# Optimization experiments

Hardware: AMD Instinct MI355X
Metric: run time of the kernel (lower is better)

The kernel has to match this reference:

```python
import jax, jax.numpy as jnp
import numpy as np

B, S, E, H, D = 4, 2048, 1024, 16, 64   # batch, seq, embed, heads, head_dim
NUM_BUCKETS, MAX_DISTANCE = 32, 128


def _relative_position_bucket(relative_position, num_buckets, max_distance):
    # causal T5-style bucketing
    max_exact = num_buckets // 2
    max_distance = max(max_distance, max_exact + 1)
    distance = jnp.maximum(-relative_position, 0)
    is_small = distance < max_exact
    safe_distance = jnp.maximum(distance, 1)
    log_scale = jnp.log(safe_distance / max_exact) / jnp.log(max_distance / max_exact)
    large_bucket = max_exact + (log_scale * (num_buckets - max_exact)).astype(jnp.int32)
    large_bucket = jnp.minimum(large_bucket, num_buckets - 1)
    return jnp.where(is_small, distance, large_bucket)


def setup_inputs() -> dict:
    key = jax.random.key(0)
    ks = jax.random.split(key, 7)
    w_scale = 1.0 / np.sqrt(E)
    inputs_q = jax.random.normal(ks[0], (B, S, E), jnp.float32)
    inputs_kv = jax.random.normal(ks[1], (B, S, E), jnp.float32)
    Wq = jax.random.normal(ks[2], (E, H * D), jnp.float32) * w_scale
    Wk = jax.random.normal(ks[3], (E, H * D), jnp.float32) * w_scale
    Wv = jax.random.normal(ks[4], (E, H * D), jnp.float32) * w_scale
    Wo = jax.random.normal(ks[5], (H * D, E), jnp.float32) * (1.0 / np.sqrt(H * D))
    rel_bias = jax.random.normal(ks[6], (H, NUM_BUCKETS), jnp.float32) * 0.02
    mask = jnp.tril(jnp.ones((S, S), dtype=bool))[None, None]  # [1,1,Q,K] causal
    return {"inputs_q": inputs_q, "inputs_kv": inputs_kv, "mask": mask,
            "Wq": Wq, "Wk": Wk, "Wv": Wv, "Wo": Wo, "rel_bias": rel_bias}


def reference(inputs_q, inputs_kv, mask, Wq, Wk, Wv, Wo, rel_bias):
    batch, q_len, embed = inputs_q.shape
    k_len = inputs_kv.shape[1]
    q = (inputs_q @ Wq).reshape(batch, q_len, H, D)
    k = (inputs_kv @ Wk).reshape(batch, k_len, H, D)
    v = (inputs_kv @ Wv).reshape(batch, k_len, H, D)
    attention = jnp.einsum("bqhd,bkhd->bhqk", q, k) * (1.0 / jnp.sqrt(D))
    # T5 relative position bias
    rel_pos = jnp.arange(k_len, dtype=jnp.int32)[None, :] - jnp.arange(q_len, dtype=jnp.int32)[:, None]
    bucket = _relative_position_bucket(rel_pos, NUM_BUCKETS, MAX_DISTANCE)  # [Q,K]
    attention = attention + jnp.take(rel_bias, bucket, axis=1)[None]  # [1,H,Q,K]
    attention = jnp.where(mask, attention, jnp.finfo(jnp.float32).min)
    normalized = jax.nn.softmax(attention, axis=-1)
    output = jnp.einsum("bhqk,bkhd->bqhd", normalized, v).reshape(batch, q_len, H * D)
    return output @ Wo
```

## Files before the change

kernel.cpp:

```cpp
#include <hip/hip_runtime.h>

typedef unsigned short u16;
typedef unsigned int u32;
typedef __bf16 bf16x8 __attribute__((ext_vector_type(8)));
typedef float f32x4 __attribute__((ext_vector_type(4)));
typedef float f32x16 __attribute__((ext_vector_type(16)));

#define S_LEN 2048
#define EMB 1024
#define NH 16
#define HD 64
#define LOG2E 1.44269504088896f

__device__ __forceinline__ u16 f2bf(float f) {
  union { float f; unsigned u; } v; v.f = f;
  unsigned r = (v.u + 0x7fffu + ((v.u >> 16) & 1u)) >> 16;
  return (u16)r;
}

__device__ __forceinline__ u32 packbf(float a, float b) {
  union { __bf16 h[2]; u32 u; } x;
  x.h[0] = (__bf16)a; x.h[1] = (__bf16)b;
  return x.u;
}

__device__ __forceinline__ void g2l16(const void* g, void* l) {
  __builtin_amdgcn_global_load_lds(
      (const unsigned int __attribute__((address_space(1)))*)g,
      (unsigned int __attribute__((address_space(3)))*)l, 16, 0, 0);
}

__device__ __forceinline__ void permswap_f(float a, float b, float& x, float& y) {
  auto r = __builtin_amdgcn_permlane32_swap(__float_as_int(a), __float_as_int(b), false, false);
  x = __int_as_float(r[0]);
  y = __int_as_float(r[1]);
}


__global__ void cvt_bf16(const float* __restrict__ src, u16* __restrict__ dst, int n4) {
  int i = blockIdx.x * blockDim.x + threadIdx.x;
  if (i < n4) {
    float4 f = ((const float4*)src)[i];
    ushort4 o;
    o.x = f2bf(f.x); o.y = f2bf(f.y); o.z = f2bf(f.z); o.w = f2bf(f.w);
    ((ushort4*)dst)[i] = o;
  }
}

__global__ void transcvt(const float* __restrict__ W, u16* __restrict__ Wt) {
  __shared__ float t[32][33];
  int k0 = blockIdx.x * 32, n0 = blockIdx.y * 32;
  int tx = threadIdx.x & 31, ty = threadIdx.x >> 5;
#pragma unroll
  for (int i = 0; i < 4; i++) t[ty + i * 8][tx] = W[(k0 + ty + i * 8) * 1024 + n0 + tx];
  __syncthreads();
#pragma unroll
  for (int i = 0; i < 4; i++) Wt[(n0 + ty + i * 8) * 1024 + k0 + tx] = f2bf(t[tx][ty + i * 8]);
}

__global__ void build_bias(const float* __restrict__ rel, float* __restrict__ tbl) {
  int i = blockIdx.x * 256 + threadIdx.x;
  int h = i >> 11, dist = i & 2047;
  int bk;
  if (dist < 16) {
    bk = dist;
  } else {
    float ls = logf((float)dist * (1.0f / 16.0f)) * (1.0f / logf(8.0f));
    bk = 16 + (int)(ls * 16.0f);
    if (bk > 31) bk = 31;
  }
  tbl[i] = rel[h * 32 + bk];
}


template <int MODE>
__global__ __launch_bounds__(256, 2) void gemm_bf16(const u16* __restrict__ A,
                                                    const u16* __restrict__ Bt,
                                                    void* __restrict__ C, float scale) {
  constexpr int K = EMB;
  __shared__ u16 As[2][128 * 32];
  __shared__ u16 Bs[2][128 * 32];
  const int m0 = blockIdx.y * 128;
  const int n0 = blockIdx.x * 128;
  const int tid = threadIdx.x;
  const int lane = tid & 63;
  const int wid = tid >> 6;
  const int wm = (wid >> 1) * 64;
  const int wn = (wid & 1) * 64;
  const int la = lane & 15;
  const int lg = lane >> 4;

  const int r0 = tid >> 2;
  const int c0 = ((tid & 3) ^ (r0 & 3)) * 8;
  const u16* gA = A + (size_t)(m0 + r0) * K + c0;
  const u16* gB = Bt + (size_t)(n0 + r0) * K + c0;

  f32x4 acc[4][4] = {};

  g2l16(gA, As[0] + tid * 8);
  g2l16(gA + 64 * K, As[0] + tid * 8 + 2048);
  g2l16(gB, Bs[0] + tid * 8);
  g2l16(gB + 64 * K, Bs[0] + tid * 8 + 2048);
  gA += 32;
  gB += 32;

  for (int t = 0; t < 32; ++t) {
    const int cur = t & 1;
    if (t < 31) {
      u16* lA = As[cur ^ 1] + tid * 8;
      u16* lB = Bs[cur ^ 1] + tid * 8;
      g2l16(gA, lA);
      g2l16(gA + 64 * K, lA + 2048);
      g2l16(gB, lB);
      g2l16(gB + 64 * K, lB + 2048);
      gA += 32;
      gB += 32;
      asm volatile("s_waitcnt vmcnt(4)" ::: "memory");
    } else {
      asm volatile("s_waitcnt vmcnt(0)" ::: "memory");
    }
    __builtin_amdgcn_s_barrier();
    asm volatile("" ::: "memory");

    bf16x8 af[4], bb[4];
#pragma unroll
    for (int mf = 0; mf < 4; mf++) {
      int row = wm + mf * 16 + la;
      af[mf] = *(const bf16x8*)&As[cur][row * 32 + ((lg ^ (row & 3)) << 3)];
    }
#pragma unroll
    for (int nf = 0; nf < 4; nf++) {
      int row = wn + nf * 16 + la;
      bb[nf] = *(const bf16x8*)&Bs[cur][row * 32 + ((lg ^ (row & 3)) << 3)];
    }
#pragma unroll
    for (int mf = 0; mf < 4; mf++)
#pragma unroll
      for (int nf = 0; nf < 4; nf++)
        acc[mf][nf] =
            __builtin_amdgcn_mfma_f32_16x16x32_bf16(af[mf], bb[nf], acc[mf][nf], 0, 0, 0);

    asm volatile("" ::: "memory");
    __builtin_amdgcn_s_barrier();
    asm volatile("" ::: "memory");
  }

#pragma unroll
  for (int mf = 0; mf < 4; mf++)
#pragma unroll
    for (int nf = 0; nf < 4; nf++)
#pragma unroll
      for (int r = 0; r < 4; r++) {
        int m = m0 + wm + mf * 16 + lg * 4 + r;
        int n = n0 + wn + nf * 16 + la;
        float v = acc[mf][nf][r] * scale;
        if constexpr (MODE == 0) {
          int b = m >> 11, s = m & 2047, h = n >> 6, d = n & 63;
          ((u16*)C)[(((size_t)(b * 16 + h) * 2048 + s) << 6) + d] = f2bf(v);
        } else if constexpr (MODE == 1) {
          int b = m >> 11, s = m & 2047, h = n >> 6, d = n & 63;
          ((u16*)C)[(((size_t)(b * 16 + h) * 64 + d) << 11) + s] = f2bf(v);
        } else {
          ((float*)C)[(size_t)m * 1024 + n] = v;
        }
      }
}


__global__ __launch_bounds__(256, 2) void attn_kernel(const u16* __restrict__ Qb,
                                                      const u16* __restrict__ Kb,
                                                      const u16* __restrict__ Vtb,
                                                      const float* __restrict__ btbl,
                                                      u16* __restrict__ O) {
  __shared__ u16 Ks[2][64 * 64];
  __shared__ u16 Vs[2][64 * 64];
  __shared__ float bias_s[S_LEN];

  const int bh = blockIdx.x;
  const int h = bh & (NH - 1);
  const int b = bh >> 4;
  const int qt = 15 - blockIdx.y;
  const int q0 = qt * 128;
  const int tid = threadIdx.x;
  const int lane = tid & 63;
  const int w = tid >> 6;
  const int la = lane & 31;
  const int hi = lane >> 5;

  {
    const float4* src = (const float4*)(btbl + h * S_LEN);
    float4* dst = (float4*)bias_s;
    dst[tid] = src[tid];
    dst[tid + 256] = src[tid + 256];
  }

  const u16* Qg = Qb + (size_t)bh * S_LEN * HD;
  const u16* Kg = Kb + (size_t)bh * S_LEN * HD;
  const u16* Vg = Vtb + (size_t)bh * HD * S_LEN;

  const int qw = q0 + w * 32;
  const int q = qw + la;

  bf16x8 qfrag[4];
#pragma unroll
  for (int kk = 0; kk < 4; kk++)
    qfrag[kk] = *(const bf16x8*)&Qg[(size_t)q * HD + kk * 16 + hi * 8];

  f32x16 oacc[2] = {};
  float mrun = -1e30f;
  float lrun = 0.f;

  const int sr = tid >> 3;
  const int scz = ((tid & 7) ^ (sr & 7)) * 8;
  const u16* kp = Kg + sr * 64 + scz;
  const u16* vp = Vg + (size_t)sr * S_LEN + scz;

  const int ntblk = (q0 + 128) >> 6;
  const int qmax = qw + 31;

  g2l16(kp, Ks[0] + tid * 8);
  g2l16(kp + 32 * 64, Ks[0] + tid * 8 + 2048);
  g2l16(vp, Vs[0] + tid * 8);
  g2l16(vp + 32 * S_LEN, Vs[0] + tid * 8 + 2048);
  kp += 4096;
  vp += 64;
  __syncthreads();

  const float bias31 = bias_s[S_LEN - 1];

  for (int t = 0; t < ntblk; ++t) {
    const int cur = t & 1;
    if (t + 1 < ntblk) {
      u16* lK = Ks[cur ^ 1] + tid * 8;
      u16* lV = Vs[cur ^ 1] + tid * 8;
      g2l16(kp, lK);
      g2l16(kp + 32 * 64, lK + 2048);
      g2l16(vp, lV);
      g2l16(vp + 32 * S_LEN, lV + 2048);
      kp += 4096;
      vp += 64;
      asm volatile("s_waitcnt vmcnt(4)" ::: "memory");
    } else {
      asm volatile("s_waitcnt vmcnt(0)" ::: "memory");
    }
    __builtin_amdgcn_s_barrier();
    asm volatile("" ::: "memory");

    const int kv0 = t << 6;
    if (kv0 <= qmax) {
      f32x16 sacc[2] = {};
      __builtin_amdgcn_s_setprio(1);
#pragma unroll
      for (int kk = 0; kk < 4; kk++) {
#pragma unroll
        for (int nf = 0; nf < 2; nf++) {
          int row = nf * 32 + la;
          bf16x8 kf = *(const bf16x8*)&Ks[cur][row * 64 + (((kk * 2 + hi) ^ (row & 7)) << 3)];
          sacc[nf] = __builtin_amdgcn_mfma_f32_32x32x16_bf16(kf, qfrag[kk], sacc[nf], 0, 0, 0);
        }
      }
      __builtin_amdgcn_s_setprio(0);

      float pf[32];
      float adde = 0.f;
      if (kv0 + 176 <= qw) {
#pragma unroll
        for (int nf = 0; nf < 2; nf++)
#pragma unroll
          for (int r = 0; r < 16; r++) pf[nf * 16 + r] = sacc[nf][r];
        adde = bias31;
      } else {
        const int qb2 = q - kv0 - 4 * hi;
        const float* bp = bias_s + (qb2 - 59);
        if (kv0 + 63 <= qw) {
#pragma unroll
          for (int nf = 0; nf < 2; nf++)
#pragma unroll
            for (int r = 0; r < 16; r++) {
              const int Cn = nf * 32 + (r & 3) + ((r >> 2) << 3);
              pf[nf * 16 + r] = sacc[nf][r] + bp[59 - Cn];
            }
        } else {
#pragma unroll
          for (int nf = 0; nf < 2; nf++)
#pragma unroll
            for (int r = 0; r < 16; r++) {
              const int Cn = nf * 32 + (r & 3) + ((r >> 2) << 3);
              pf[nf * 16 + r] = (Cn <= qb2) ? (sacc[nf][r] + bp[59 - Cn]) : -1e30f;
            }
        }
      }

      float a[11];
#pragma unroll
      for (int i = 0; i < 10; i++)
        a[i] = fmaxf(fmaxf(pf[3 * i], pf[3 * i + 1]), pf[3 * i + 2]);
      a[10] = fmaxf(pf[30], pf[31]);
      float b0 = fmaxf(fmaxf(a[0], a[1]), a[2]);
      float b1 = fmaxf(fmaxf(a[3], a[4]), a[5]);
      float b2 = fmaxf(fmaxf(a[6], a[7]), a[8]);
      float b3 = fmaxf(a[9], a[10]);
      float mt = fmaxf(fmaxf(b0, b1), fmaxf(b2, b3)) + adde;
      {
        float x, y;
        permswap_f(mt, mt, x, y);
        mt = fmaxf(x, y);
      }

      if (__any(mt > mrun + 8.0f)) {
        float mn = fmaxf(mrun, mt);
        float sc = exp2f((mrun - mn) * LOG2E);
        mrun = mn;
        lrun *= sc;
        oacc[0] *= sc;
        oacc[1] *= sc;
      }
      const float ec = (adde - mrun) * LOG2E;

      float ps[16];
#pragma unroll
      for (int i = 0; i < 16; i++) {
        float p0 = exp2f(fmaf(pf[i], LOG2E, ec));
        float p1 = exp2f(fmaf(pf[i + 16], LOG2E, ec));
        pf[i] = p0;
        pf[i + 16] = p1;
        ps[i] = p0 + p1;
      }
#pragma unroll
      for (int i = 0; i < 8; i++) ps[i] += ps[i + 8];
#pragma unroll
      for (int i = 0; i < 4; i++) ps[i] += ps[i + 4];
      float rs = (ps[0] + ps[1]) + (ps[2] + ps[3]);
      {
        float x, y;
        permswap_f(rs, rs, x, y);
        rs = x + y;
      }
      lrun += rs;

      u32 paw[4][4];
#pragma unroll
      for (int ks = 0; ks < 4; ks++) {
        const int nf = ks >> 1;
        const int e80 = (ks & 1) * 2;
#pragma unroll
        for (int half = 0; half < 2; half++) {
          u32 Y0 = packbf(pf[nf * 16 + 4 * e80 + 2 * half], pf[nf * 16 + 4 * e80 + 2 * half + 1]);
          u32 Y1 = packbf(pf[nf * 16 + 4 * (e80 + 1) + 2 * half],
                          pf[nf * 16 + 4 * (e80 + 1) + 2 * half + 1]);
          auto r = __builtin_amdgcn_permlane32_swap((int)Y0, (int)Y1, false, false);
          paw[ks][half] = (u32)r[0];
          paw[ks][2 + half] = (u32)r[1];
        }
      }

      __builtin_amdgcn_s_setprio(1);
#pragma unroll
      for (int d2 = 0; d2 < 2; d2++) {
#pragma unroll
        for (int ks = 0; ks < 4; ks++) {
          int row = d2 * 32 + la;
          bf16x8 vf = *(const bf16x8*)&Vs[cur][row * 64 + (((ks * 2 + hi) ^ (row & 7)) << 3)];
          union { u32 w[4]; bf16x8 v; } pu;
          pu.w[0] = paw[ks][0]; pu.w[1] = paw[ks][1];
          pu.w[2] = paw[ks][2]; pu.w[3] = paw[ks][3];
          oacc[d2] = __builtin_amdgcn_mfma_f32_32x32x16_bf16(vf, pu.v, oacc[d2], 0, 0, 0);
        }
      }
      __builtin_amdgcn_s_setprio(0);
    }

    asm volatile("" ::: "memory");
    __builtin_amdgcn_s_barrier();
    asm volatile("" ::: "memory");
  }

  const float inv = 1.0f / lrun;
  u16* Og = O + ((size_t)(b * S_LEN + q)) * EMB + h * HD;
#pragma unroll
  for (int d2 = 0; d2 < 2; d2++)
#pragma unroll
    for (int g = 0; g < 4; g++) {
      ushort4 ov;
      ov.x = f2bf(oacc[d2][g * 4 + 0] * inv);
      ov.y = f2bf(oacc[d2][g * 4 + 1] * inv);
      ov.z = f2bf(oacc[d2][g * 4 + 2] * inv);
      ov.w = f2bf(oacc[d2][g * 4 + 3] * inv);
      *(ushort4*)&Og[d2 * 32 + g * 8 + hi * 4] = ov;
    }
}


extern "C" void kernel_launch(void* const* d_in, const int* in_sizes, int n_in, void* d_out,
                              int out_size, void* d_ws, size_t ws_size, hipStream_t stream) {
  (void)in_sizes; (void)n_in; (void)out_size; (void)ws_size;
  const float* inq = (const float*)d_in[0];
  const float* inkv = (const float*)d_in[1];
  const float* Wq = (const float*)d_in[3];
  const float* Wk = (const float*)d_in[4];
  const float* Wv = (const float*)d_in[5];
  const float* Wo = (const float*)d_in[6];
  const float* rel = (const float*)d_in[7];
  float* out = (float*)d_out;

  char* ws = (char*)d_ws;
  size_t off = 0;
  auto alloc = [&](size_t bytes) {
    void* p = ws + off;
    off += (bytes + 255) & ~(size_t)255;
    return p;
  };
  u16* Aq = (u16*)alloc(16777216);
  u16* Akv = (u16*)alloc(16777216);
  u16* Wqt = (u16*)alloc(2097152);
  u16* Wkt = (u16*)alloc(2097152);
  u16* Wvt = (u16*)alloc(2097152);
  u16* Wot = (u16*)alloc(2097152);
  u16* Qb = (u16*)alloc(16777216);
  u16* Kb = (u16*)alloc(16777216);
  u16* Vtb = (u16*)alloc(16777216);
  u16* Ob = (u16*)alloc(16777216);
  float* btbl = (float*)alloc(131072);

  cvt_bf16<<<8192, 256, 0, stream>>>(inq, Aq, 2097152);
  cvt_bf16<<<8192, 256, 0, stream>>>(inkv, Akv, 2097152);
  transcvt<<<dim3(32, 32), 256, 0, stream>>>(Wq, Wqt);
  transcvt<<<dim3(32, 32), 256, 0, stream>>>(Wk, Wkt);
  transcvt<<<dim3(32, 32), 256, 0, stream>>>(Wv, Wvt);
  transcvt<<<dim3(32, 32), 256, 0, stream>>>(Wo, Wot);
  build_bias<<<128, 256, 0, stream>>>(rel, btbl);

  gemm_bf16<0><<<dim3(8, 64), 256, 0, stream>>>(Aq, Wqt, Qb, 0.125f);
  gemm_bf16<0><<<dim3(8, 64), 256, 0, stream>>>(Akv, Wkt, Kb, 1.0f);
  gemm_bf16<1><<<dim3(8, 64), 256, 0, stream>>>(Akv, Wvt, Vtb, 1.0f);
  attn_kernel<<<dim3(64, 16), 256, 0, stream>>>(Qb, Kb, Vtb, btbl, Ob);
  gemm_bf16<2><<<dim3(8, 64), 256, 0, stream>>>(Ob, Wot, out, 1.0f);
}
```

Measured before the change: 225.8 us.

## Fuse QKV GEMMs, fold log2e into scales, packed softmax, unroll attention loop

The three Q/K/V projection GEMMs become a single launch over concatenated transposed weights, which fills more of the GPU in one grid. The softmax scale and the bias table are pre-multiplied by log2e so the exponentials need no extra FMA, the rescale threshold is adjusted to match, and the softmax reductions use packed two-wide float ops. The attention tile loop is manually unrolled by two with compile-time buffer indices. The GEMMs drop their double-buffered LDS prefetch for a simple single-buffer load-then-sync loop, which may expose global-load latency.

```diff
diff --git a/kernel.cpp b/kernel.cpp
--- a/kernel.cpp
+++ b/kernel.cpp
@@ -3,6 +3,7 @@
 typedef unsigned short u16;
 typedef unsigned int u32;
 typedef __bf16 bf16x8 __attribute__((ext_vector_type(8)));
+typedef float f32x2 __attribute__((ext_vector_type(2)));
 typedef float f32x4 __attribute__((ext_vector_type(4)));
 typedef float f32x16 __attribute__((ext_vector_type(16)));
 
@@ -11,6 +12,8 @@
 #define NH 16
 #define HD 64
 #define LOG2E 1.44269504088896f
+#define QSCALE (0.125f * LOG2E)
+#define THRL 11.5415603f
 
 __device__ __forceinline__ u16 f2bf(float f) {
   union { float f; unsigned u; } v; v.f = f;
@@ -30,10 +33,13 @@
       (unsigned int __attribute__((address_space(3)))*)l, 16, 0, 0);
 }
 
-__device__ __forceinline__ void permswap_f(float a, float b, float& x, float& y) {
-  auto r = __builtin_amdgcn_permlane32_swap(__float_as_int(a), __float_as_int(b), false, false);
-  x = __int_as_float(r[0]);
-  y = __int_as_float(r[1]);
+__device__ __forceinline__ float permswap_max(float a) {
+  auto r = __builtin_amdgcn_permlane32_swap(__float_as_int(a), __float_as_int(a), false, false);
+  return fmaxf(__int_as_float(r[0]), __int_as_float(r[1]));
+}
+__device__ __forceinline__ float permswap_add(float a) {
+  auto r = __builtin_amdgcn_permlane32_swap(__float_as_int(a), __float_as_int(a), false, false);
+  return __int_as_float(r[0]) + __int_as_float(r[1]);
 }
 
 
@@ -69,17 +75,92 @@
     bk = 16 + (int)(ls * 16.0f);
     if (bk > 31) bk = 31;
   }
-  tbl[i] = rel[h * 32 + bk];
-}
-
-
-template <int MODE>
-__global__ __launch_bounds__(256, 2) void gemm_bf16(const u16* __restrict__ A,
-                                                    const u16* __restrict__ Bt,
-                                                    void* __restrict__ C, float scale) {
+  tbl[i] = rel[h * 32 + bk] * LOG2E;
+}
+
+
+__global__ __launch_bounds__(256, 2) void gemm_qkv(const u16* __restrict__ Aq,
+                                                   const u16* __restrict__ Akv,
+                                                   const u16* __restrict__ Wt,
+                                                   u16* __restrict__ QKV, float qscale) {
   constexpr int K = EMB;
-  __shared__ u16 As[2][128 * 32];
-  __shared__ u16 Bs[2][128 * 32];
+  __shared__ u16 As[128 * 32];
+  __shared__ u16 Bs[128 * 32];
+  const int m0 = blockIdx.y * 128;
+  const int n0 = blockIdx.x * 128;
+  const int mat = n0 >> 10;
+  const u16* A = (mat == 0) ? Aq : Akv;
+  const int tid = threadIdx.x;
+  const int lane = tid & 63;
+  const int wid = tid >> 6;
+  const int wm = (wid >> 1) * 64;
+  const int wn = (wid & 1) * 64;
+  const int la = lane & 15;
+  const int lg = lane >> 4;
+
+  const int r0 = tid >> 2;
+  const int c0 = ((tid & 3) ^ (r0 & 3)) * 8;
+  const u16* gA = A + (size_t)(m0 + r0) * K + c0;
+  const u16* gB = Wt + (size_t)(n0 + r0) * K + c0;
+  u16* lA = As + tid * 8;
+  u16* lB = Bs + tid * 8;
+
+  f32x4 acc[4][4] = {};
+
+  for (int k0 = 0; k0 < K; k0 += 32) {
+    g2l16(gA, lA);
+    g2l16(gA + 64 * K, lA + 2048);
+    g2l16(gB, lB);
+    g2l16(gB + 64 * K, lB + 2048);
+    gA += 32;
+    gB += 32;
+    __syncthreads();
+    bf16x8 af[4], bb[4];
+#pragma unroll
+    for (int mf = 0; mf < 4; mf++) {
+      int row = wm + mf * 16 + la;
+      af[mf] = *(const bf16x8*)&As[row * 32 + ((lg ^ (row & 3)) << 3)];
+    }
+#pragma unroll
+    for (int nf = 0; nf < 4; nf++) {
+      int row = wn + nf * 16 + la;
+      bb[nf] = *(const bf16x8*)&Bs[row * 32 + ((lg ^ (row & 3)) << 3)];
+    }
+#pragma unroll
+    for (int mf = 0; mf < 4; mf++)
+#pragma unroll
+      for (int nf = 0; nf < 4; nf++)
+        acc[mf][nf] =
+            __builtin_amdgcn_mfma_f32_16x16x32_bf16(af[mf], bb[nf], acc[mf][nf], 0, 0, 0);
+    __syncthreads();
+  }
+
+  const float sc = (mat == 0) ? qscale : 1.0f;
+#pragma unroll
+  for (int mf = 0; mf < 4; mf++)
+#pragma unroll
+    for (int nf = 0; nf < 4; nf++)
+#pragma unroll
+      for (int r = 0; r < 4; r++) {
+        int m = m0 + wm + mf * 16 + lg * 4 + r;
+        int n = n0 + wn + nf * 16 + la;
+        float v = acc[mf][nf][r] * sc;
+        int b = m >> 11, s = m & 2047, h = (n >> 6) & 15, d = n & 63;
+        size_t base = (size_t)mat << 23;
+        if (mat < 2)
+          QKV[base + (((size_t)(b * 16 + h) * 2048 + s) << 6) + d] = f2bf(v);
+        else
+          QKV[base + (((size_t)(b * 16 + h) * 64 + d) << 11) + s] = f2bf(v);
+      }
+}
+
+
+__global__ __launch_bounds__(256, 2) void gemm_out(const u16* __restrict__ A,
+                                                   const u16* __restrict__ Bt,
+                                                   float* __restrict__ C) {
+  constexpr int K = EMB;
+  __shared__ u16 As[128 * 32];
+  __shared__ u16 Bs[128 * 32];
   const int m0 = blockIdx.y * 128;
   const int n0 = blockIdx.x * 128;
   const int tid = threadIdx.x;
@@ -94,44 +175,29 @@
   const int c0 = ((tid & 3) ^ (r0 & 3)) * 8;
   const u16* gA = A + (size_t)(m0 + r0) * K + c0;
   const u16* gB = Bt + (size_t)(n0 + r0) * K + c0;
+  u16* lA = As + tid * 8;
+  u16* lB = Bs + tid * 8;
 
   f32x4 acc[4][4] = {};
 
-  g2l16(gA, As[0] + tid * 8);
-  g2l16(gA + 64 * K, As[0] + tid * 8 + 2048);
-  g2l16(gB, Bs[0] + tid * 8);
-  g2l16(gB + 64 * K, Bs[0] + tid * 8 + 2048);
-  gA += 32;
-  gB += 32;
-
-  for (int t = 0; t < 32; ++t) {
-    const int cur = t & 1;
-    if (t < 31) {
-      u16* lA = As[cur ^ 1] + tid * 8;
-      u16* lB = Bs[cur ^ 1] + tid * 8;
-      g2l16(gA, lA);
-      g2l16(gA + 64 * K, lA + 2048);
-      g2l16(gB, lB);
-      g2l16(gB + 64 * K, lB + 2048);
-      gA += 32;
-      gB += 32;
-      asm volatile("s_waitcnt vmcnt(4)" ::: "memory");
-    } else {
-      asm volatile("s_waitcnt vmcnt(0)" ::: "memory");
-    }
-    __builtin_amdgcn_s_barrier();
-    asm volatile("" ::: "memory");
-
+  for (int k0 = 0; k0 < K; k0 += 32) {
+    g2l16(gA, lA);
+    g2l16(gA + 64 * K, lA + 2048);
+    g2l16(gB, lB);
+    g2l16(gB + 64 * K, lB + 2048);
+    gA += 32;
+    gB += 32;
+    __syncthreads();
     bf16x8 af[4], bb[4];
 #pragma unroll
     for (int mf = 0; mf < 4; mf++) {
       int row = wm + mf * 16 + la;
-      af[mf] = *(const bf16x8*)&As[cur][row * 32 + ((lg ^ (row & 3)) << 3)];
+      af[mf] = *(const bf16x8*)&As[row * 32 + ((lg ^ (row & 3)) << 3)];
     }
 #pragma unroll
     for (int nf = 0; nf < 4; nf++) {
       int row = wn + nf * 16 + la;
-      bb[nf] = *(const bf16x8*)&Bs[cur][row * 32 + ((lg ^ (row & 3)) << 3)];
+      bb[nf] = *(const bf16x8*)&Bs[row * 32 + ((lg ^ (row & 3)) << 3)];
     }
 #pragma unroll
     for (int mf = 0; mf < 4; mf++)
@@ -139,10 +205,7 @@
       for (int nf = 0; nf < 4; nf++)
         acc[mf][nf] =
             __builtin_amdgcn_mfma_f32_16x16x32_bf16(af[mf], bb[nf], acc[mf][nf], 0, 0, 0);
-
-    asm volatile("" ::: "memory");
-    __builtin_amdgcn_s_barrier();
-    asm volatile("" ::: "memory");
+    __syncthreads();
   }
 
 #pragma unroll
@@ -153,19 +216,155 @@
       for (int r = 0; r < 4; r++) {
         int m = m0 + wm + mf * 16 + lg * 4 + r;
         int n = n0 + wn + nf * 16 + la;
-        float v = acc[mf][nf][r] * scale;
-        if constexpr (MODE == 0) {
-          int b = m >> 11, s = m & 2047, h = n >> 6, d = n & 63;
-          ((u16*)C)[(((size_t)(b * 16 + h) * 2048 + s) << 6) + d] = f2bf(v);
-        } else if constexpr (MODE == 1) {
-          int b = m >> 11, s = m & 2047, h = n >> 6, d = n & 63;
-          ((u16*)C)[(((size_t)(b * 16 + h) * 64 + d) << 11) + s] = f2bf(v);
-        } else {
-          ((float*)C)[(size_t)m * 1024 + n] = v;
-        }
+        C[(size_t)m * 1024 + n] = acc[mf][nf][r];
       }
 }
 
+
+__device__ __forceinline__ void softmax_repack(const f32x16* sacc, int kv0, int qw, int q, int hi,
+                                               const float* bias_s, float bias31, float& mrun,
+                                               float& lrun, f32x16& o0, f32x16& o1,
+                                               u32 (&paw)[4][4]) {
+  f32x2 pf[16];
+  float adde = 0.f;
+  if (kv0 + 176 <= qw) {
+#pragma unroll
+    for (int j = 0; j < 16; j++) {
+      const int nf = j >> 3, r = (j & 7) * 2;
+      pf[j] = (f32x2){sacc[nf][r], sacc[nf][r + 1]};
+    }
+    adde = bias31;
+  } else {
+    const int qb2 = q - kv0 - 4 * hi;
+    const float* bp = bias_s + (qb2 - 59);
+    if (kv0 + 63 <= qw) {
+#pragma unroll
+      for (int j = 0; j < 16; j++) {
+        const int nf = j >> 3, r = (j & 7) * 2;
+        const int Cn = nf * 32 + (r & 3) + ((r >> 2) << 3);
+        f32x2 bv = {bp[59 - Cn], bp[58 - Cn]};
+        pf[j] = (f32x2){sacc[nf][r], sacc[nf][r + 1]} + bv;
+      }
+    } else {
+#pragma unroll
+      for (int j = 0; j < 16; j++) {
+        const int nf = j >> 3, r = (j & 7) * 2;
+        const int Cn = nf * 32 + (r & 3) + ((r >> 2) << 3);
+        pf[j].x = (Cn <= qb2) ? (sacc[nf][r] + bp[59 - Cn]) : -1e30f;
+        pf[j].y = (Cn + 1 <= qb2) ? (sacc[nf][r + 1] + bp[58 - Cn]) : -1e30f;
+      }
+    }
+  }
+
+  f32x2 t8[8];
+#pragma unroll
+  for (int i = 0; i < 8; i++) t8[i] = __builtin_elementwise_max(pf[i], pf[i + 8]);
+#pragma unroll
+  for (int i = 0; i < 4; i++) t8[i] = __builtin_elementwise_max(t8[i], t8[i + 4]);
+  f32x2 m2 = __builtin_elementwise_max(__builtin_elementwise_max(t8[0], t8[1]),
+                                       __builtin_elementwise_max(t8[2], t8[3]));
+  float mt = fmaxf(m2.x, m2.y) + adde;
+  mt = permswap_max(mt);
+
+  if (__any(mt > mrun + THRL)) {
+    float mn = fmaxf(mrun, mt);
+    float s = exp2f(mrun - mn);
+    mrun = mn;
+    lrun *= s;
+    o0 *= s;
+    o1 *= s;
+  }
+  const f32x2 ec2 = {adde - mrun, adde - mrun};
+
+  f32x2 s8[8];
+#pragma unroll
+  for (int j = 0; j < 16; j++) {
+    f32x2 a = pf[j] + ec2;
+    f32x2 p = {exp2f(a.x), exp2f(a.y)};
+    pf[j] = p;
+    if (j < 8) s8[j] = p;
+    else s8[j - 8] += p;
+  }
+#pragma unroll
+  for (int i = 0; i < 4; i++) s8[i] += s8[i + 4];
+  f32x2 s2 = (s8[0] + s8[1]) + (s8[2] + s8[3]);
+  lrun += permswap_add(s2.x + s2.y);
+
+#pragma unroll
+  for (int ks = 0; ks < 4; ks++) {
+    const int j0b = (ks >> 1) * 8 + (ks & 1) * 4;
+#pragma unroll
+    for (int half = 0; half < 2; half++) {
+      u32 Y0 = packbf(pf[j0b + half].x, pf[j0b + half].y);
+      u32 Y1 = packbf(pf[j0b + 2 + half].x, pf[j0b + 2 + half].y);
+      auto r = __builtin_amdgcn_permlane32_swap((int)Y0, (int)Y1, false, false);
+      paw[ks][half] = (u32)r[0];
+      paw[ks][2 + half] = (u32)r[1];
+    }
+  }
+}
+
+template <int CUR>
+__device__ __forceinline__ void tile_body(int t, int ntblk, int qmax, int qw, int q, int hi,
+                                          int la, int tid, const u16*& kp, const u16*& vp,
+                                          u16 (*Ks)[64 * 64], u16 (*Vs)[64 * 64],
+                                          const bf16x8 (&qfrag)[4], const float* bias_s,
+                                          float bias31, float& mrun, float& lrun, f32x16& o0,
+                                          f32x16& o1) {
+  if (t + 1 < ntblk) {
+    u16* lK = Ks[CUR ^ 1] + tid * 8;
+    u16* lV = Vs[CUR ^ 1] + tid * 8;
+    g2l16(kp, lK);
+    g2l16(kp + 32 * 64, lK + 2048);
+    g2l16(vp, lV);
+    g2l16(vp + 32 * S_LEN, lV + 2048);
+    kp += 4096;
+    vp += 64;
+    asm volatile("s_waitcnt vmcnt(4)" ::: "memory");
+  } else {
+    asm volatile("s_waitcnt vmcnt(0)" ::: "memory");
+  }
+  __builtin_amdgcn_s_barrier();
+  asm volatile("" ::: "memory");
+
+  const int kv0 = t << 6;
+  if (kv0 <= qmax) {
+    f32x16 sacc[2] = {};
+    __builtin_amdgcn_s_setprio(1);
+#pragma unroll
+    for (int kk = 0; kk < 4; kk++)
+#pragma unroll
+      for (int nf = 0; nf < 2; nf++) {
+        int row = nf * 32 + la;
+        bf16x8 kf = *(const bf16x8*)&Ks[CUR][row * 64 + (((kk * 2 + hi) ^ (row & 7)) << 3)];
+        sacc[nf] = __builtin_amdgcn_mfma_f32_32x32x16_bf16(kf, qfrag[kk], sacc[nf], 0, 0, 0);
+      }
+    __builtin_amdgcn_s_setprio(0);
+
+    u32 paw[4][4];
+    softmax_repack(sacc, kv0, qw, q, hi, bias_s, bias31, mrun, lrun, o0, o1, paw);
+
+    __builtin_amdgcn_s_setprio(1);
+#pragma unroll
+    for (int d2 = 0; d2 < 2; d2++) {
+      f32x16& oa = d2 ? o1 : o0;
+#pragma unroll
+      for (int ks = 0; ks < 4; ks++) {
+        int row = d2 * 32 + la;
+        bf16x8 vf = *(const bf16x8*)&Vs[CUR][row * 64 + (((ks * 2 + hi) ^ (row & 7)) << 3)];
+        union { u32 w[4]; bf16x8 v; } pu;
+        pu.w[0] = paw[ks][0]; pu.w[1] = paw[ks][1];
+        pu.w[2] = paw[ks][2]; pu.w[3] = paw[ks][3];
+        oa = __builtin_amdgcn_mfma_f32_32x32x16_bf16(vf, pu.v, oa, 0, 0, 0);
+      }
+    }
+    __builtin_amdgcn_s_setprio(0);
+  }
+
+  asm volatile("" ::: "memory");
+  __builtin_amdgcn_s_barrier();
+  asm volatile("" ::: "memory");
+}
 
 __global__ __launch_bounds__(256, 2) void attn_kernel(const u16* __restrict__ Qb,
                                                       const u16* __restrict__ Kb,
@@ -206,7 +405,7 @@
   for (int kk = 0; kk < 4; kk++)
     qfrag[kk] = *(const bf16x8*)&Qg[(size_t)q * HD + kk * 16 + hi * 8];
 
-  f32x16 oacc[2] = {};
+  f32x16 o0 = {}, o1 = {};
   float mrun = -1e30f;
   float lrun = 0.f;
 
@@ -224,170 +423,37 @@
   g2l16(vp + 32 * S_LEN, Vs[0] + tid * 8 + 2048);
   kp += 4096;
   vp += 64;
-  __syncthreads();
+  asm volatile("s_waitcnt lgkmcnt(0)" ::: "memory");
+  __builtin_amdgcn_s_barrier();
+  asm volatile("" ::: "memory");
 
   const float bias31 = bias_s[S_LEN - 1];
 
-  for (int t = 0; t < ntblk; ++t) {
-    const int cur = t & 1;
-    if (t + 1 < ntblk) {
-      u16* lK = Ks[cur ^ 1] + tid * 8;
-      u16* lV = Vs[cur ^ 1] + tid * 8;
-      g2l16(kp, lK);
-      g2l16(kp + 32 * 64, lK + 2048);
-      g2l16(vp, lV);
-      g2l16(vp + 32 * S_LEN, lV + 2048);
-      kp += 4096;
-      vp += 64;
-      asm volatile("s_waitcnt vmcnt(4)" ::: "memory");
-    } else {
-      asm volatile("s_waitcnt vmcnt(0)" ::: "memory");
-    }
-    __builtin_amdgcn_s_barrier();
-    asm volatile("" ::: "memory");
-
-    const int kv0 = t << 6;
-    if (kv0 <= qmax) {
-      f32x16 sacc[2] = {};
-      __builtin_amdgcn_s_setprio(1);
-#pragma unroll
-      for (int kk = 0; kk < 4; kk++) {
-#pragma unroll
-        for (int nf = 0; nf < 2; nf++) {
-          int row = nf * 32 + la;
-          bf16x8 kf = *(const bf16x8*)&Ks[cur][row * 64 + (((kk * 2 + hi) ^ (row & 7)) << 3)];
-          sacc[nf] = __builtin_amdgcn_mfma_f32_32x32x16_bf16(kf, qfrag[kk], sacc[nf], 0, 0, 0);
-        }
-      }
-      __builtin_amdgcn_s_setprio(0);
-
-      float pf[32];
-      float adde = 0.f;
-      if (kv0 + 176 <= qw) {
-#pragma unroll
-        for (int nf = 0; nf < 2; nf++)
-#pragma unroll
-          for (int r = 0; r < 16; r++) pf[nf * 16 + r] = sacc[nf][r];
-        adde = bias31;
-      } else {
-        const int qb2 = q - kv0 - 4 * hi;
-        const float* bp = bias_s + (qb2 - 59);
-        if (kv0 + 63 <= qw) {
-#pragma unroll
-          for (int nf = 0; nf < 2; nf++)
-#pragma unroll
-            for (int r = 0; r < 16; r++) {
-              const int Cn = nf * 32 + (r & 3) + ((r >> 2) << 3);
-              pf[nf * 16 + r] = sacc[nf][r] + bp[59 - Cn];
-            }
-        } else {
-#pragma unroll
-          for (int nf = 0; nf < 2; nf++)
-#pragma unroll
-            for (int r = 0; r < 16; r++) {
-              const int Cn = nf * 32 + (r & 3) + ((r >> 2) << 3);
-              pf[nf * 16 + r] = (Cn <= qb2) ? (sacc[nf][r] + bp[59 - Cn]) : -1e30f;
-            }
-        }
-      }
-
-      float a[11];
-#pragma unroll
-      for (int i = 0; i < 10; i++)
-        a[i] = fmaxf(fmaxf(pf[3 * i], pf[3 * i + 1]), pf[3 * i + 2]);
-      a[10] = fmaxf(pf[30], pf[31]);
-      float b0 = fmaxf(fmaxf(a[0], a[1]), a[2]);
-      float b1 = fmaxf(fmaxf(a[3], a[4]), a[5]);
-      float b2 = fmaxf(fmaxf(a[6], a[7]), a[8]);
-      float b3 = fmaxf(a[9], a[10]);
-      float mt = fmaxf(fmaxf(b0, b1), fmaxf(b2, b3)) + adde;
-      {
-        float x, y;
-        permswap_f(mt, mt, x, y);
-        mt = fmaxf(x, y);
-      }
-
-      if (__any(mt > mrun + 8.0f)) {
-        float mn = fmaxf(mrun, mt);
-        float sc = exp2f((mrun - mn) * LOG2E);
-        mrun = mn;
-        lrun *= sc;
-        oacc[0] *= sc;
-        oacc[1] *= sc;
-      }
-      const float ec = (adde - mrun) * LOG2E;
-
-      float ps[16];
-#pragma unroll
-      for (int i = 0; i < 16; i++) {
-        float p0 = exp2f(fmaf(pf[i], LOG2E, ec));
-        float p1 = exp2f(fmaf(pf[i + 16], LOG2E, ec));
-        pf[i] = p0;
-        pf[i + 16] = p1;
-        ps[i] = p0 + p1;
-      }
-#pragma unroll
-      for (int i = 0; i < 8; i++) ps[i] += ps[i + 8];
-#pragma unroll
-      for (int i = 0; i < 4; i++) ps[i] += ps[i + 4];
-      float rs = (ps[0] + ps[1]) + (ps[2] + ps[3]);
-      {
-        float x, y;
-        permswap_f(rs, rs, x, y);
-        rs = x + y;
-      }
-      lrun += rs;
-
-      u32 paw[4][4];
-#pragma unroll
-      for (int ks = 0; ks < 4; ks++) {
-        const int nf = ks >> 1;
-        const int e80 = (ks & 1) * 2;
-#pragma unroll
-        for (int half = 0; half < 2; half++) {
-          u32 Y0 = packbf(pf[nf * 16 + 4 * e80 + 2 * half], pf[nf * 16 + 4 * e80 + 2 * half + 1]);
-          u32 Y1 = packbf(pf[nf * 16 + 4 * (e80 + 1) + 2 * half],
-                          pf[nf * 16 + 4 * (e80 + 1) + 2 * half + 1]);
-          auto r = __builtin_amdgcn_permlane32_swap((int)Y0, (int)Y1, false, false);
-          paw[ks][half] = (u32)r[0];
-          paw[ks][2 + half] = (u32)r[1];
-        }
-      }
-
-      __builtin_amdgcn_s_setprio(1);
-#pragma unroll
-      for (int d2 = 0; d2 < 2; d2++) {
-#pragma unroll
-        for (int ks = 0; ks < 4; ks++) {
-          int row = d2 * 32 + la;
-          bf16x8 vf = *(const bf16x8*)&Vs[cur][row * 64 + (((ks * 2 + hi) ^ (row & 7)) << 3)];
-          union { u32 w[4]; bf16x8 v; } pu;
-          pu.w[0] = paw[ks][0]; pu.w[1] = paw[ks][1];
-          pu.w[2] = paw[ks][2]; pu.w[3] = paw[ks][3];
-          oacc[d2] = __builtin_amdgcn_mfma_f32_32x32x16_bf16(vf, pu.v, oacc[d2], 0, 0, 0);
-        }
-      }
-      __builtin_amdgcn_s_setprio(0);
-    }
-
-    asm volatile("" ::: "memory");
-    __builtin_amdgcn_s_barrier();
-    asm volatile("" ::: "memory");
+  int t = 0;
+  while (t < ntblk) {
+    tile_body<0>(t, ntblk, qmax, qw, q, hi, la, tid, kp, vp, Ks, Vs, qfrag, bias_s, bias31,
+                 mrun, lrun, o0, o1);
+    ++t;
+    tile_body<1>(t, ntblk, qmax, qw, q, hi, la, tid, kp, vp, Ks, Vs, qfrag, bias_s, bias31,
+                 mrun, lrun, o0, o1);
+    ++t;
   }
 
   const float inv = 1.0f / lrun;
   u16* Og = O + ((size_t)(b * S_LEN + q)) * EMB + h * HD;
 #pragma unroll
-  for (int d2 = 0; d2 < 2; d2++)
+  for (int d2 = 0; d2 < 2; d2++) {
+    const f32x16& oa = d2 ? o1 : o0;
 #pragma unroll
     for (int g = 0; g < 4; g++) {
       ushort4 ov;
-      ov.x = f2bf(oacc[d2][g * 4 + 0] * inv);
-      ov.y = f2bf(oacc[d2][g * 4 + 1] * inv);
-      ov.z = f2bf(oacc[d2][g * 4 + 2] * inv);
-      ov.w = f2bf(oacc[d2][g * 4 + 3] * inv);
+      ov.x = f2bf(oa[g * 4 + 0] * inv);
+      ov.y = f2bf(oa[g * 4 + 1] * inv);
+      ov.z = f2bf(oa[g * 4 + 2] * inv);
+      ov.w = f2bf(oa[g * 4 + 3] * inv);
       *(ushort4*)&Og[d2 * 32 + g * 8 + hi * 4] = ov;
     }
+  }
 }
 
 
@@ -412,27 +478,25 @@
   };
   u16* Aq = (u16*)alloc(16777216);
   u16* Akv = (u16*)alloc(16777216);
-  u16* Wqt = (u16*)alloc(2097152);
-  u16* Wkt = (u16*)alloc(2097152);
-  u16* Wvt = (u16*)alloc(2097152);
+  u16* Wqkvt = (u16*)alloc(6291456);
   u16* Wot = (u16*)alloc(2097152);
-  u16* Qb = (u16*)alloc(16777216);
-  u16* Kb = (u16*)alloc(16777216);
-  u16* Vtb = (u16*)alloc(16777216);
+  u16* QKV = (u16*)alloc(50331648);
   u16* Ob = (u16*)alloc(16777216);
   float* btbl = (float*)alloc(131072);
 
+  u16* Qb = QKV;
+  u16* Kb = QKV + 8388608;
+  u16* Vtb = QKV + 16777216;
+
   cvt_bf16<<<8192, 256, 0, stream>>>(inq, Aq, 2097152);
   cvt_bf16<<<8192, 256, 0, stream>>>(inkv, Akv, 2097152);
-  transcvt<<<dim3(32, 32), 256, 0, stream>>>(Wq, Wqt);
-  transcvt<<<dim3(32, 32), 256, 0, stream>>>(Wk, Wkt);
-  transcvt<<<dim3(32, 32), 256, 0, stream>>>(Wv, Wvt);
+  transcvt<<<dim3(32, 32), 256, 0, stream>>>(Wq, Wqkvt);
+  transcvt<<<dim3(32, 32), 256, 0, stream>>>(Wk, Wqkvt + 1048576);
+  transcvt<<<dim3(32, 32), 256, 0, stream>>>(Wv, Wqkvt + 2097152);
   transcvt<<<dim3(32, 32), 256, 0, stream>>>(Wo, Wot);
   build_bias<<<128, 256, 0, stream>>>(rel, btbl);
 
-  gemm_bf16<0><<<dim3(8, 64), 256, 0, stream>>>(Aq, Wqt, Qb, 0.125f);
-  gemm_bf16<0><<<dim3(8, 64), 256, 0, stream>>>(Akv, Wkt, Kb, 1.0f);
-  gemm_bf16<1><<<dim3(8, 64), 256, 0, stream>>>(Akv, Wvt, Vtb, 1.0f);
+  gemm_qkv<<<dim3(24, 64), 256, 0, stream>>>(Aq, Akv, Wqkvt, QKV, QSCALE);
   attn_kernel<<<dim3(64, 16), 256, 0, stream>>>(Qb, Kb, Vtb, btbl, Ob);
-  gemm_bf16<2><<<dim3(8, 64), 256, 0, stream>>>(Ob, Wot, out, 1.0f);
-}
+  gemm_out<<<dim3(8, 64), 256, 0, stream>>>(Ob, Wot, out);
+}
```

Measured after the change: 228.6 us. About the same (+1.3%).
